# Kernel optimization log

Measured on AMD Instinct MI355X. Metric: run time of the kernel, lower is better.

Reference implementation:

```python
import jax, jax.numpy as jnp
import numpy as np

EPS = 1e-5

def gn(x, gamma, beta):
    # GroupNorm(num_groups=1) on [N, C]: normalize over channel dim per row
    m = x.mean(-1, keepdims=True)
    v = ((x - m) ** 2).mean(-1, keepdims=True)
    return (x - m) * jax.lax.rsqrt(v + EPS) * gamma + beta

def setup_inputs() -> dict:
    key = jax.random.key(0)
    N, M, E, D = 50000, 50000, 500000, 128
    ks = jax.random.split(key, 32)
    s = 0.05
    inp = {
        'agts': jax.random.normal(ks[0], (N, D), jnp.float32),
        'ctx': jax.random.normal(ks[1], (M, D), jnp.float32),
        'agt_ctrs': jax.random.normal(ks[2], (N, 2), jnp.float32),
        'ctx_ctrs': jax.random.normal(ks[3], (M, 2), jnp.float32),
        'hi': jax.random.randint(ks[4], (E,), 0, N, jnp.int32),
        'wi': jax.random.randint(ks[5], (E,), 0, M, jnp.int32),
        # dist MLP: Linear(2,D,bias) -> ReLU -> Linear(D,D,nobias)+GN+ReLU
        'W_d1': jax.random.normal(ks[6], (2, D), jnp.float32) * s,
        'b_d1': jnp.zeros((D,), jnp.float32),
        'W_d2': jax.random.normal(ks[7], (D, D), jnp.float32) * s,
        'g_d2': jnp.ones((D,), jnp.float32),
        'b_d2': jnp.zeros((D,), jnp.float32),
        # query: Linear(D,D,nobias)+GN+ReLU
        'W_q': jax.random.normal(ks[8], (D, D), jnp.float32) * s,
        'g_q': jnp.ones((D,), jnp.float32),
        'b_q': jnp.zeros((D,), jnp.float32),
        # ctx MLP: Linear(3D,D,nobias)+GN+ReLU -> Linear(D,D,nobias)
        'W_c1': jax.random.normal(ks[9], (3 * D, D), jnp.float32) * s,
        'g_c1': jnp.ones((D,), jnp.float32),
        'b_c1': jnp.zeros((D,), jnp.float32),
        'W_c2': jax.random.normal(ks[10], (D, D), jnp.float32) * s,
        # agt linear (nobias), post-scatter GN, final Linear(D,D,nobias)+GN (no act)
        'W_a': jax.random.normal(ks[11], (D, D), jnp.float32) * s,
        'g_n': jnp.ones((D,), jnp.float32),
        'b_n': jnp.zeros((D,), jnp.float32),
        'W_l': jax.random.normal(ks[12], (D, D), jnp.float32) * s,
        'g_l': jnp.ones((D,), jnp.float32),
        'b_l': jnp.zeros((D,), jnp.float32),
    }
    return inp

def reference(agts, ctx, agt_ctrs, ctx_ctrs, hi, wi,
              W_d1, b_d1, W_d2, g_d2, b_d2,
              W_q, g_q, b_q,
              W_c1, g_c1, b_c1, W_c2,
              W_a, g_n, b_n, W_l, g_l, b_l):
    res = agts
    # gather per-edge relative distances and embed
    dist = agt_ctrs[hi] - ctx_ctrs[wi]                      # [E, 2]
    d = jax.nn.relu(dist @ W_d1 + b_d1)                     # [E, D]
    d = jax.nn.relu(gn(d @ W_d2, g_d2, b_d2))               # [E, D]
    # per-edge agent query
    q = jax.nn.relu(gn(agts[hi] @ W_q, g_q, b_q))           # [E, D]
    # concat(dist_emb, query, gathered ctx) -> message MLP
    msg = jnp.concatenate([d, q, ctx[wi]], axis=-1)         # [E, 3D]
    msg = jax.nn.relu(gn(msg @ W_c1, g_c1, b_c1)) @ W_c2    # [E, D]
    # transform agents and scatter-add messages
    a = agts @ W_a
    a = a.at[hi].add(msg)
    a = jax.nn.relu(gn(a, g_n, b_n))
    a = gn(a @ W_l, g_l, b_l)   # act=False
    a = jax.nn.relu(a + res)
    return a
```

## Files before the change

### kernel.cpp

```cpp
#include <hip/hip_runtime.h>
#include <hip/hip_bf16.h>
#include <stdint.h>


typedef __bf16 bfx8 __attribute__((ext_vector_type(8)));
typedef float f32x4 __attribute__((ext_vector_type(4)));
typedef short s16x2 __attribute__((ext_vector_type(2)));

__device__ __forceinline__ unsigned short f2bfu(float f) {
  unsigned u = __builtin_bit_cast(unsigned, f);
  return (unsigned short)((u + 0x7fffu + ((u >> 16) & 1u)) >> 16);
}
__device__ __forceinline__ float bfu2f(unsigned short u) {
  return __builtin_bit_cast(float, ((unsigned)u) << 16);
}
__device__ __forceinline__ unsigned pk2(unsigned x, unsigned y) {
  float lo = bfu2f((unsigned short)(x & 0xffffu)) + bfu2f((unsigned short)(y & 0xffffu));
  float hi = bfu2f((unsigned short)(x >> 16)) + bfu2f((unsigned short)(y >> 16));
  return (unsigned)f2bfu(lo) | ((unsigned)f2bfu(hi) << 16);
}

__device__ __forceinline__ void atomAddBf2(unsigned short* p, unsigned v) {
#if defined(__has_builtin) && __has_builtin(__builtin_amdgcn_global_atomic_fadd_v2bf16)
  __builtin_amdgcn_global_atomic_fadd_v2bf16(
      (__attribute__((address_space(1))) s16x2*)p, __builtin_bit_cast(s16x2, v));
#else
  unsigned* q = (unsigned*)p;
  unsigned old = *q;
  while (true) {
    unsigned nv = pk2(old, v);
    unsigned prev = atomicCAS(q, old, nv);
    if (prev == old) break;
    old = prev;
  }
#endif
}

__device__ __forceinline__ int swzb(int row, int kbyte) {
  return (row * 256 + kbyte) ^ ((row & 7) << 4);
}

__device__ __forceinline__ void stage_w(const unsigned short* wsrc, char* dst, int tid, int nth) {
  const uint4* s = (const uint4*)wsrc;
  uint4* d = (uint4*)dst;
  for (int i = tid; i < 2048; i += nth) d[i] = s[i];
}

template <bool A_FROM_LDS>
__device__ __forceinline__ void wave_gemm(const char* WtL, const char* XL,
                                          const bfx8* aF, f32x4 acc[8],
                                          int lg, int lr) {
#pragma unroll
  for (int ks = 0; ks < 4; ++ks) {
    bfx8 a;
    if (A_FROM_LDS)
      a = *(const bfx8*)(XL + swzb(lr, (ks * 32 + lg * 8) * 2));
    else
      a = aF[ks];
#pragma unroll
    for (int t = 0; t < 8; ++t) {
      int n = t * 16 + lr;
      bfx8 b = *(const bfx8*)(WtL + swzb(n, (ks * 32 + lg * 8) * 2));
      acc[t] = __builtin_amdgcn_mfma_f32_16x16x32_bf16(a, b, acc[t], 0, 0, 0);
    }
  }
}

__device__ __forceinline__ void wave_gn(f32x4 acc[8], const float* g, const float* b,
                                        int lg, int lr, bool do_relu) {
  float s0 = 0.f, s1 = 0.f, s2 = 0.f, s3 = 0.f;
  float q0 = 0.f, q1 = 0.f, q2 = 0.f, q3 = 0.f;
#pragma unroll
  for (int t = 0; t < 8; ++t) {
    float v0 = acc[t][0], v1 = acc[t][1], v2 = acc[t][2], v3 = acc[t][3];
    s0 += v0; q0 += v0 * v0;
    s1 += v1; q1 += v1 * v1;
    s2 += v2; q2 += v2 * v2;
    s3 += v3; q3 += v3 * v3;
  }
#pragma unroll
  for (int m = 1; m <= 8; m <<= 1) {
    s0 += __shfl_xor(s0, m, 64); q0 += __shfl_xor(q0, m, 64);
    s1 += __shfl_xor(s1, m, 64); q1 += __shfl_xor(q1, m, 64);
    s2 += __shfl_xor(s2, m, 64); q2 += __shfl_xor(q2, m, 64);
    s3 += __shfl_xor(s3, m, 64); q3 += __shfl_xor(q3, m, 64);
  }
  float gc[8], bc[8];
#pragma unroll
  for (int t = 0; t < 8; ++t) { gc[t] = g[t * 16 + lr]; bc[t] = b[t * 16 + lr]; }
  float mean[4], rstd[4];
  {
    const float inv = 1.f / 128.f;
    float m0 = s0 * inv, m1 = s1 * inv, m2 = s2 * inv, m3 = s3 * inv;
    mean[0] = m0; mean[1] = m1; mean[2] = m2; mean[3] = m3;
    rstd[0] = rsqrtf(q0 * inv - m0 * m0 + 1e-5f);
    rstd[1] = rsqrtf(q1 * inv - m1 * m1 + 1e-5f);
    rstd[2] = rsqrtf(q2 * inv - m2 * m2 + 1e-5f);
    rstd[3] = rsqrtf(q3 * inv - m3 * m3 + 1e-5f);
  }
#pragma unroll
  for (int t = 0; t < 8; ++t) {
#pragma unroll
    for (int r = 0; r < 4; ++r) {
      float v = (acc[t][r] - mean[r]) * rstd[r] * gc[t] + bc[t];
      if (do_relu) v = fmaxf(v, 0.f);
      acc[t][r] = v;
    }
  }
}

__device__ __forceinline__ void wave_stage(char* XL, const f32x4 acc[8], int lg, int lr) {
#pragma unroll
  for (int t = 0; t < 8; ++t) {
#pragma unroll
    for (int r = 0; r < 4; ++r) {
      int row = 4 * lg + r, c = t * 16 + lr;
      *(unsigned short*)(XL + swzb(row, 2 * c)) = f2bfu(acc[t][r]);
    }
  }
}

__global__ void k_prep_weights(const float* Wd2, const float* Wc1, const float* Wc2,
                               const float* Wq, const float* Wa, const float* Wl,
                               unsigned short* wsW) {
  __shared__ unsigned short tmp[128 * 128];
  int m = blockIdx.x;
  const float* src;
  switch (m) {
    case 0: src = Wd2; break;
    case 1: src = Wc1; break;
    case 2: src = Wc1 + 128 * 128; break;
    case 3: src = Wc1 + 256 * 128; break;
    case 4: src = Wc2; break;
    case 5: src = Wq; break;
    case 6: src = Wa; break;
    default: src = Wl; break;
  }
  int tid = threadIdx.x;
#pragma unroll
  for (int i = 0; i < 16; ++i) {
    int lin = i * 256 + tid;
    float4 v = ((const float4*)src)[lin];
    ushort4 b;
    b.x = f2bfu(v.x); b.y = f2bfu(v.y); b.z = f2bfu(v.z); b.w = f2bfu(v.w);
    *(ushort4*)&tmp[lin * 4] = b;
  }
  __syncthreads();
  unsigned short* dst = wsW + (size_t)m * 16384;
#pragma unroll
  for (int i = 0; i < 16; ++i) {
    int lin = i * 256 + tid;
    int n = lin >> 5, q = lin & 31, k0 = q * 4;
    ushort4 b;
    b.x = tmp[(k0 + 0) * 128 + n];
    b.y = tmp[(k0 + 1) * 128 + n];
    b.z = tmp[(k0 + 2) * 128 + n];
    b.w = tmp[(k0 + 3) * 128 + n];
    *(ushort4*)((char*)dst + swzb(n, k0 * 2)) = b;
  }
}

__global__ void k_hist(const int* hi, int* cnt, int E) {
  int e = blockIdx.x * 256 + threadIdx.x;
  if (e < E) atomicAdd(&cnt[hi[e]], 1);
}

__global__ __launch_bounds__(1024) void k_scan(const int* cnt, int* cur, int N) {
  __shared__ int part[1024];
  int tid = threadIdx.x;
  int C = (N + 1023) >> 10;
  int b0 = tid * C, b1 = b0 + C; if (b1 > N) b1 = N; if (b0 > N) b0 = N;
  int s = 0;
  for (int i = b0; i < b1; ++i) s += cnt[i];
  part[tid] = s;
  __syncthreads();
  for (int d = 1; d < 1024; d <<= 1) {
    int v = (tid >= d) ? part[tid - d] : 0;
    __syncthreads();
    part[tid] += v;
    __syncthreads();
  }
  int excl = (tid == 0) ? 0 : part[tid - 1];
  for (int i = b0; i < b1; ++i) {
    cur[i] = excl;
    excl += cnt[i];
  }
}

__global__ void k_fill(const int* hi, const int* wi, int* cur,
                       int* hi_s, int* wi_s, int E) {
  int e = blockIdx.x * 256 + threadIdx.x;
  if (e < E) {
    int h = hi[e];
    int p = atomicAdd(&cur[h], 1);
    hi_s[p] = h;
    wi_s[p] = wi[e];
  }
}

__global__ __launch_bounds__(256, 2) void k_ctx(const float* ctx, const unsigned short* wsW,
                                                unsigned short* cc, int M) {
  __shared__ __align__(16) char lds[32768];
  int tid = threadIdx.x, wid = tid >> 6, lane = tid & 63, lg = lane >> 4, lr = lane & 15;
  int base = blockIdx.x * 64;
  stage_w(wsW + 3 * 16384, lds, tid, 256);
  int row = base + 16 * wid + lr;
  int rload = row < M ? row : M - 1;
  bfx8 cf[4];
#pragma unroll
  for (int ks = 0; ks < 4; ++ks) {
    int k0 = ks * 32 + lg * 8;
    const float4* p = (const float4*)&ctx[(size_t)rload * 128 + k0];
    float4 a = p[0], b = p[1];
    bfx8 f;
    f[0] = (__bf16)a.x; f[1] = (__bf16)a.y; f[2] = (__bf16)a.z; f[3] = (__bf16)a.w;
    f[4] = (__bf16)b.x; f[5] = (__bf16)b.y; f[6] = (__bf16)b.z; f[7] = (__bf16)b.w;
    cf[ks] = f;
  }
  __syncthreads();
  f32x4 acc[8];
#pragma unroll
  for (int t = 0; t < 8; ++t) acc[t] = 0.f;
  wave_gemm<false>(lds, nullptr, cf, acc, lg, lr);
#pragma unroll
  for (int r = 0; r < 4; ++r) {
    int grow = base + 16 * wid + 4 * lg + r;
    if (grow < M) {
#pragma unroll
      for (int t = 0; t < 8; ++t)
        cc[(size_t)grow * 128 + t * 16 + lr] = f2bfu(acc[t][r]);
    }
  }
}

__global__ __launch_bounds__(768, 3) void k_agents(const float* agts, const float* g_q,
                                                   const float* b_q, const unsigned short* wsW,
                                                   unsigned short* qc, int N) {
  __shared__ __align__(16) char lds[114688];
  char* WqL = lds;
  char* WcL = lds + 32768;
  int tid = threadIdx.x, wid = tid >> 6, lane = tid & 63, lg = lane >> 4, lr = lane & 15;
  char* actL = lds + 65536 + wid * 4096;
  stage_w(wsW + 5 * 16384, WqL, tid, 768);
  stage_w(wsW + 2 * 16384, WcL, tid, 768);
  __syncthreads();
  int nTiles = (N + 15) >> 4;
  int stride = gridDim.x * 12;
  for (int tile = blockIdx.x * 12 + wid; tile < nTiles; tile += stride) {
    int base = tile << 4;
    int row = base + lr; if (row >= N) row = N - 1;
    bfx8 af[4];
#pragma unroll
    for (int ks = 0; ks < 4; ++ks) {
      int k0 = ks * 32 + lg * 8;
      const float4* p = (const float4*)&agts[(size_t)row * 128 + k0];
      float4 a = p[0], b = p[1];
      bfx8 f;
      f[0] = (__bf16)a.x; f[1] = (__bf16)a.y; f[2] = (__bf16)a.z; f[3] = (__bf16)a.w;
      f[4] = (__bf16)b.x; f[5] = (__bf16)b.y; f[6] = (__bf16)b.z; f[7] = (__bf16)b.w;
      af[ks] = f;
    }
    f32x4 acc[8];
#pragma unroll
    for (int t = 0; t < 8; ++t) acc[t] = 0.f;
    wave_gemm<false>(WqL, nullptr, af, acc, lg, lr);
    wave_gn(acc, g_q, b_q, lg, lr, true);
    wave_stage(actL, acc, lg, lr);
#pragma unroll
    for (int t = 0; t < 8; ++t) acc[t] = 0.f;
    wave_gemm<true>(WcL, actL, nullptr, acc, lg, lr);
#pragma unroll
    for (int r = 0; r < 4; ++r) {
      int grow = base + 4 * lg + r;
      if (grow < N) {
#pragma unroll
        for (int t = 0; t < 8; ++t)
          qc[(size_t)grow * 128 + t * 16 + lr] = f2bfu(acc[t][r]);
      }
    }
  }
}

__global__ __launch_bounds__(768, 3) void k_edge(
    const float* agt_ctrs, const float* ctx_ctrs, const int* hi_s, const int* wi_s,
    const float* W_d1, const float* b_d1, const float* g_d2, const float* b_d2,
    const float* g_c1, const float* b_c1, const unsigned short* wsW,
    const unsigned short* qc, const unsigned short* cc, unsigned short* S, int E) {
  __shared__ __align__(16) char lds[163840];
  char* Wd2L = lds;
  char* Wc1L = lds + 32768;
  int tid = threadIdx.x, wid = tid >> 6, lane = tid & 63, lg = lane >> 4, lr = lane & 15;
  char* region = lds + 65536 + wid * 8192;
  char* QCCL = region;
  char* actL = region + 4096;
  float* hB = (float*)region;
  stage_w(wsW + 0 * 16384, Wd2L, tid, 768);
  stage_w(wsW + 1 * 16384, Wc1L, tid, 768);
  __syncthreads();
  int nTiles = (E + 15) >> 4;
  int stride = gridDim.x * 12;
  for (int tile = blockIdx.x * 12 + wid; tile < nTiles; tile += stride) {
    int base = tile << 4;
    {
      int gr = lane >> 2, gq = lane & 3;
      int ge = base + gr; if (ge >= E) ge = E - 1;
      int gh = hi_s[ge], gw2 = wi_s[ge];
      const uint4* qrow = (const uint4*)(qc + (size_t)gh * 128) + gq * 4;
      const uint4* crow = (const uint4*)(cc + (size_t)gw2 * 128) + gq * 4;
#pragma unroll
      for (int i = 0; i < 4; ++i) {
        uint4 av = qrow[i], bv = crow[i];
        uint4 o;
        o.x = pk2(av.x, bv.x); o.y = pk2(av.y, bv.y);
        o.z = pk2(av.z, bv.z); o.w = pk2(av.w, bv.w);
        *(uint4*)(QCCL + swzb(gr, gq * 64 + i * 16)) = o;
      }
    }
    bfx8 d1f[4];
    {
      int e1 = base + lr; if (e1 >= E) e1 = E - 1;
      int h1 = hi_s[e1], w1 = wi_s[e1];
      float dx = agt_ctrs[2 * h1] - ctx_ctrs[2 * w1];
      float dy = agt_ctrs[2 * h1 + 1] - ctx_ctrs[2 * w1 + 1];
#pragma unroll
      for (int ks = 0; ks < 4; ++ks) {
        int k0 = ks * 32 + lg * 8;
        const float4* w0 = (const float4*)&W_d1[k0];
        const float4* w1p = (const float4*)&W_d1[128 + k0];
        const float4* bp = (const float4*)&b_d1[k0];
        float4 w0a = w0[0], w0b = w0[1];
        float4 w1a = w1p[0], w1b = w1p[1];
        float4 ba = bp[0], bb = bp[1];
        bfx8 f;
        f[0] = (__bf16)fmaxf(dx * w0a.x + dy * w1a.x + ba.x, 0.f);
        f[1] = (__bf16)fmaxf(dx * w0a.y + dy * w1a.y + ba.y, 0.f);
        f[2] = (__bf16)fmaxf(dx * w0a.z + dy * w1a.z + ba.z, 0.f);
        f[3] = (__bf16)fmaxf(dx * w0a.w + dy * w1a.w + ba.w, 0.f);
        f[4] = (__bf16)fmaxf(dx * w0b.x + dy * w1b.x + bb.x, 0.f);
        f[5] = (__bf16)fmaxf(dx * w0b.y + dy * w1b.y + bb.y, 0.f);
        f[6] = (__bf16)fmaxf(dx * w0b.z + dy * w1b.z + bb.z, 0.f);
        f[7] = (__bf16)fmaxf(dx * w0b.w + dy * w1b.w + bb.w, 0.f);
        d1f[ks] = f;
      }
    }
    f32x4 acc[8];
#pragma unroll
    for (int t = 0; t < 8; ++t) acc[t] = 0.f;
    wave_gemm<false>(Wd2L, nullptr, d1f, acc, lg, lr);
    wave_gn(acc, g_d2, b_d2, lg, lr, true);
    wave_stage(actL, acc, lg, lr);
#pragma unroll
    for (int t = 0; t < 8; ++t) {
#pragma unroll
      for (int r = 0; r < 4; ++r)
        acc[t][r] = bfu2f(*(const unsigned short*)(QCCL + swzb(4 * lg + r, 2 * (16 * t + lr))));
    }
    wave_gemm<true>(Wc1L, actL, nullptr, acc, lg, lr);
    wave_gn(acc, g_c1, b_c1, lg, lr, true);
#pragma unroll
    for (int t = 0; t < 8; ++t) {
#pragma unroll
      for (int r = 0; r < 4; ++r)
        hB[(4 * lg + r) * 128 + 16 * t + lr] = acc[t][r];
    }
    {
      int nprev = (base > 0) ? hi_s[base - 1] : -1;
      int nnext = (base + 16 < E) ? hi_s[base + 16] : -1;
      int curn = -1, seg_start = 0;
      float s0 = 0.f, s1 = 0.f;
#pragma unroll
      for (int r = 0; r <= 16; ++r) {
        int n;
        if (r < 16) {
          int sl = base + r;
          n = (sl < E) ? hi_s[sl] : -1;
        } else {
          n = -2;
        }
        if (n != curn) {
          if (curn >= 0) {
            bool atomS = (seg_start == 0) && (curn == nprev);
            bool atomE = (r == 16) && (curn == nnext);
            unsigned pkv = (unsigned)f2bfu(s0) | ((unsigned)f2bfu(s1) << 16);
            unsigned short* addr = S + (size_t)curn * 128 + 2 * lane;
            if (atomS || atomE) atomAddBf2(addr, pkv);
            else *(unsigned*)addr = pkv;
          }
          curn = n; seg_start = r; s0 = 0.f; s1 = 0.f;
        }
        if (r < 16 && n >= 0) {
          float2 hv = *(const float2*)(hB + r * 128 + 2 * lane);
          s0 += hv.x; s1 += hv.y;
        }
      }
    }
  }
}

__global__ __launch_bounds__(768, 3) void k_final(const float* agts, const float* g_n,
                                                  const float* b_n, const float* g_l,
                                                  const float* b_l, const unsigned short* wsW,
                                                  const unsigned short* S, float* out, int N) {
  __shared__ __align__(16) char lds[147456];
  char* WaL = lds;
  char* Wc2L = lds + 32768;
  char* WlL = lds + 65536;
  int tid = threadIdx.x, wid = tid >> 6, lane = tid & 63, lg = lane >> 4, lr = lane & 15;
  char* actL = lds + 98304 + wid * 4096;
  stage_w(wsW + 6 * 16384, WaL, tid, 768);
  stage_w(wsW + 4 * 16384, Wc2L, tid, 768);
  stage_w(wsW + 7 * 16384, WlL, tid, 768);
  __syncthreads();
  int nTiles = (N + 15) >> 4;
  int stride = gridDim.x * 12;
  for (int tile = blockIdx.x * 12 + wid; tile < nTiles; tile += stride) {
    int base = tile << 4;
    int row = base + lr; if (row >= N) row = N - 1;
    bfx8 af[4], sf[4];
#pragma unroll
    for (int ks = 0; ks < 4; ++ks) {
      int k0 = ks * 32 + lg * 8;
      const float4* p = (const float4*)&agts[(size_t)row * 128 + k0];
      float4 a = p[0], b = p[1];
      bfx8 f;
      f[0] = (__bf16)a.x; f[1] = (__bf16)a.y; f[2] = (__bf16)a.z; f[3] = (__bf16)a.w;
      f[4] = (__bf16)b.x; f[5] = (__bf16)b.y; f[6] = (__bf16)b.z; f[7] = (__bf16)b.w;
      af[ks] = f;
      sf[ks] = *(const bfx8*)&S[(size_t)row * 128 + k0];
    }
    f32x4 acc[8];
#pragma unroll
    for (int t = 0; t < 8; ++t) acc[t] = 0.f;
    wave_gemm<false>(WaL, nullptr, af, acc, lg, lr);
    wave_gemm<false>(Wc2L, nullptr, sf, acc, lg, lr);
    wave_gn(acc, g_n, b_n, lg, lr, true);
    wave_stage(actL, acc, lg, lr);
#pragma unroll
    for (int t = 0; t < 8; ++t) acc[t] = 0.f;
    wave_gemm<true>(WlL, actL, nullptr, acc, lg, lr);
    wave_gn(acc, g_l, b_l, lg, lr, false);
#pragma unroll
    for (int r = 0; r < 4; ++r) {
      int grow = base + 4 * lg + r;
      if (grow < N) {
#pragma unroll
        for (int t = 0; t < 8; ++t) {
          int c = t * 16 + lr;
          float res = agts[(size_t)grow * 128 + c];
          out[(size_t)grow * 128 + c] = fmaxf(acc[t][r] + res, 0.f);
        }
      }
    }
  }
}

extern "C" void kernel_launch(void* const* d_in, const int* in_sizes, int n_in,
                              void* d_out, int out_size, void* d_ws, size_t ws_size,
                              hipStream_t stream) {
  const float* agts = (const float*)d_in[0];
  const float* ctx = (const float*)d_in[1];
  const float* agt_ctrs = (const float*)d_in[2];
  const float* ctx_ctrs = (const float*)d_in[3];
  const int* hi = (const int*)d_in[4];
  const int* wi = (const int*)d_in[5];
  const float* W_d1 = (const float*)d_in[6];
  const float* b_d1 = (const float*)d_in[7];
  const float* W_d2 = (const float*)d_in[8];
  const float* g_d2 = (const float*)d_in[9];
  const float* b_d2 = (const float*)d_in[10];
  const float* W_q = (const float*)d_in[11];
  const float* g_q = (const float*)d_in[12];
  const float* b_q = (const float*)d_in[13];
  const float* W_c1 = (const float*)d_in[14];
  const float* g_c1 = (const float*)d_in[15];
  const float* b_c1 = (const float*)d_in[16];
  const float* W_c2 = (const float*)d_in[17];
  const float* W_a = (const float*)d_in[18];
  const float* g_n = (const float*)d_in[19];
  const float* b_n = (const float*)d_in[20];
  const float* W_l = (const float*)d_in[21];
  const float* g_l = (const float*)d_in[22];
  const float* b_l = (const float*)d_in[23];

  int N = in_sizes[0] / 128;
  int M = in_sizes[1] / 128;
  int E = in_sizes[4];

  float* out = (float*)d_out;
  char* ws = (char*)d_ws;
  size_t o = 0;
  unsigned short* qcP = (unsigned short*)(ws + o); o += (size_t)N * 256;
  unsigned short* ccP = (unsigned short*)(ws + o); o += (size_t)M * 256;
  unsigned short* Sp  = (unsigned short*)(ws + o); o += (size_t)N * 256;
  unsigned short* wsW = (unsigned short*)(ws + o); o += 262144;
  int* cnt  = (int*)(ws + o); o += ((size_t)N * 4 + 255) & ~255ull;
  int* cur  = (int*)(ws + o); o += ((size_t)N * 4 + 255) & ~255ull;
  int* hi_s = (int*)(ws + o); o += ((size_t)E * 4 + 255) & ~255ull;
  int* wi_s = (int*)(ws + o); o += ((size_t)E * 4 + 255) & ~255ull;

  hipMemsetAsync(cnt, 0, (size_t)N * 4, stream);
  hipMemsetAsync(Sp, 0, (size_t)N * 256, stream);
  k_prep_weights<<<8, 256, 0, stream>>>(W_d2, W_c1, W_c2, W_q, W_a, W_l, wsW);
  k_hist<<<(E + 255) / 256, 256, 0, stream>>>(hi, cnt, E);
  k_scan<<<1, 1024, 0, stream>>>(cnt, cur, N);
  k_fill<<<(E + 255) / 256, 256, 0, stream>>>(hi, wi, cur, hi_s, wi_s, E);
  k_ctx<<<(M + 63) / 64, 256, 0, stream>>>(ctx, wsW, ccP, M);
  k_agents<<<256, 768, 0, stream>>>(agts, g_q, b_q, wsW, qcP, N);
  k_edge<<<256, 768, 0, stream>>>(agt_ctrs, ctx_ctrs, hi_s, wi_s, W_d1, b_d1,
                                  g_d2, b_d2, g_c1, b_c1, wsW, qcP, ccP, Sp, E);
  k_final<<<256, 768, 0, stream>>>(agts, g_n, b_n, g_l, b_l, wsW, Sp, out, N);
}
```

Measured before the change: 363.5 us.

## Parallelize CSR scan, pack edge indices, and widen kernels to 1024 threads

Replaces the single-block serial scan with a three-pass multi-block scan and records per-edge ranks during the histogram. The fill step then writes sorted (h,w) pairs with plain stores instead of atomics. All main kernels move to 1024-thread blocks, and k_ctx becomes persistent. k_edge now gathers q/c values directly into registers instead of staging them through LDS, and hoists W_d1/b_d1 and the GN gamma/beta into registers once per block. The goal is to remove the serial scan bottleneck and LDS round-trips, at the cost of higher register pressure and the LDS footprint implied by the 4-blocks-per-CU launch bounds.

```diff
diff --git a/kernel.cpp b/kernel.cpp
--- a/kernel.cpp
+++ b/kernel.cpp
@@ -66,8 +66,14 @@
   }
 }
 
-__device__ __forceinline__ void wave_gn(f32x4 acc[8], const float* g, const float* b,
-                                        int lg, int lr, bool do_relu) {
+__device__ __forceinline__ void gn_cols(const float* __restrict__ g, const float* __restrict__ b,
+                                        int lr, float gc[8], float bc[8]) {
+#pragma unroll
+  for (int t = 0; t < 8; ++t) { gc[t] = g[t * 16 + lr]; bc[t] = b[t * 16 + lr]; }
+}
+
+__device__ __forceinline__ void wave_gn(f32x4 acc[8], const float gc[8], const float bc[8],
+                                        bool do_relu) {
   float s0 = 0.f, s1 = 0.f, s2 = 0.f, s3 = 0.f;
   float q0 = 0.f, q1 = 0.f, q2 = 0.f, q3 = 0.f;
 #pragma unroll
@@ -85,9 +91,6 @@
     s2 += __shfl_xor(s2, m, 64); q2 += __shfl_xor(q2, m, 64);
     s3 += __shfl_xor(s3, m, 64); q3 += __shfl_xor(q3, m, 64);
   }
-  float gc[8], bc[8];
-#pragma unroll
-  for (int t = 0; t < 8; ++t) { gc[t] = g[t * 16 + lr]; bc[t] = b[t * 16 + lr]; }
   float mean[4], rstd[4];
   {
     const float inv = 1.f / 128.f;
@@ -160,93 +163,133 @@
   }
 }
 
-__global__ void k_hist(const int* hi, int* cnt, int E) {
+__global__ void k_hist(const int* __restrict__ hi, int* cnt, int* rank, int E) {
   int e = blockIdx.x * 256 + threadIdx.x;
-  if (e < E) atomicAdd(&cnt[hi[e]], 1);
-}
-
-__global__ __launch_bounds__(1024) void k_scan(const int* cnt, int* cur, int N) {
-  __shared__ int part[1024];
-  int tid = threadIdx.x;
-  int C = (N + 1023) >> 10;
-  int b0 = tid * C, b1 = b0 + C; if (b1 > N) b1 = N; if (b0 > N) b0 = N;
+  if (e < E) rank[e] = atomicAdd(&cnt[hi[e]], 1);
+}
+
+__global__ void k_scan1(const int* __restrict__ cnt, int* bsum, int N) {
+  __shared__ int red[256];
+  int b = blockIdx.x, t = threadIdx.x;
+  int i0 = b * 1024 + t * 4;
   int s = 0;
-  for (int i = b0; i < b1; ++i) s += cnt[i];
-  part[tid] = s;
+#pragma unroll
+  for (int j = 0; j < 4; ++j) { int i = i0 + j; if (i < N) s += cnt[i]; }
+  red[t] = s;
+  __syncthreads();
+  for (int d = 128; d > 0; d >>= 1) {
+    if (t < d) red[t] += red[t + d];
+    __syncthreads();
+  }
+  if (t == 0) bsum[b] = red[0];
+}
+
+__global__ __launch_bounds__(1024) void k_scan2(int* bsum, int nb) {
+  __shared__ int sh[1024];
+  int t = threadIdx.x;
+  sh[t] = (t < nb) ? bsum[t] : 0;
   __syncthreads();
   for (int d = 1; d < 1024; d <<= 1) {
-    int v = (tid >= d) ? part[tid - d] : 0;
+    int v = (t >= d) ? sh[t - d] : 0;
     __syncthreads();
-    part[tid] += v;
+    sh[t] += v;
     __syncthreads();
   }
-  int excl = (tid == 0) ? 0 : part[tid - 1];
-  for (int i = b0; i < b1; ++i) {
-    cur[i] = excl;
-    excl += cnt[i];
-  }
-}
-
-__global__ void k_fill(const int* hi, const int* wi, int* cur,
-                       int* hi_s, int* wi_s, int E) {
+  if (t < nb) bsum[t] = (t == 0) ? 0 : sh[t - 1];
+}
+
+__global__ void k_scan3(const int* __restrict__ cnt, const int* __restrict__ bsum,
+                        int* base, int N) {
+  __shared__ int tsum[256];
+  int b = blockIdx.x, t = threadIdx.x;
+  int i0 = b * 1024 + t * 4;
+  int v[4]; int s = 0;
+#pragma unroll
+  for (int j = 0; j < 4; ++j) { int i = i0 + j; v[j] = (i < N) ? cnt[i] : 0; s += v[j]; }
+  tsum[t] = s;
+  __syncthreads();
+  for (int d = 1; d < 256; d <<= 1) {
+    int x = (t >= d) ? tsum[t - d] : 0;
+    __syncthreads();
+    tsum[t] += x;
+    __syncthreads();
+  }
+  int off = bsum[b] + ((t == 0) ? 0 : tsum[t - 1]);
+#pragma unroll
+  for (int j = 0; j < 4; ++j) {
+    int i = i0 + j;
+    if (i < N) { base[i] = off; off += v[j]; }
+  }
+}
+
+__global__ void k_fill(const int* __restrict__ hi, const int* __restrict__ wi,
+                       const int* __restrict__ base, const int* __restrict__ rank,
+                       uint2* hw, int E) {
   int e = blockIdx.x * 256 + threadIdx.x;
   if (e < E) {
     int h = hi[e];
-    int p = atomicAdd(&cur[h], 1);
-    hi_s[p] = h;
-    wi_s[p] = wi[e];
-  }
-}
-
-__global__ __launch_bounds__(256, 2) void k_ctx(const float* ctx, const unsigned short* wsW,
-                                                unsigned short* cc, int M) {
+    int p = base[h] + rank[e];
+    hw[p] = make_uint2((unsigned)h, (unsigned)wi[e]);
+  }
+}
+
+__global__ __launch_bounds__(1024, 4) void k_ctx(const float* __restrict__ ctx,
+                                                 const unsigned short* __restrict__ wsW,
+                                                 unsigned short* __restrict__ cc, int M) {
   __shared__ __align__(16) char lds[32768];
   int tid = threadIdx.x, wid = tid >> 6, lane = tid & 63, lg = lane >> 4, lr = lane & 15;
-  int base = blockIdx.x * 64;
-  stage_w(wsW + 3 * 16384, lds, tid, 256);
-  int row = base + 16 * wid + lr;
-  int rload = row < M ? row : M - 1;
-  bfx8 cf[4];
-#pragma unroll
-  for (int ks = 0; ks < 4; ++ks) {
-    int k0 = ks * 32 + lg * 8;
-    const float4* p = (const float4*)&ctx[(size_t)rload * 128 + k0];
-    float4 a = p[0], b = p[1];
-    bfx8 f;
-    f[0] = (__bf16)a.x; f[1] = (__bf16)a.y; f[2] = (__bf16)a.z; f[3] = (__bf16)a.w;
-    f[4] = (__bf16)b.x; f[5] = (__bf16)b.y; f[6] = (__bf16)b.z; f[7] = (__bf16)b.w;
-    cf[ks] = f;
-  }
-  __syncthreads();
-  f32x4 acc[8];
-#pragma unroll
-  for (int t = 0; t < 8; ++t) acc[t] = 0.f;
-  wave_gemm<false>(lds, nullptr, cf, acc, lg, lr);
-#pragma unroll
-  for (int r = 0; r < 4; ++r) {
-    int grow = base + 16 * wid + 4 * lg + r;
-    if (grow < M) {
-#pragma unroll
-      for (int t = 0; t < 8; ++t)
-        cc[(size_t)grow * 128 + t * 16 + lr] = f2bfu(acc[t][r]);
-    }
-  }
-}
-
-__global__ __launch_bounds__(768, 3) void k_agents(const float* agts, const float* g_q,
-                                                   const float* b_q, const unsigned short* wsW,
-                                                   unsigned short* qc, int N) {
-  __shared__ __align__(16) char lds[114688];
+  stage_w(wsW + 3 * 16384, lds, tid, 1024);
+  __syncthreads();
+  int nTiles = (M + 15) >> 4;
+  int stride = gridDim.x * 16;
+  for (int tile = blockIdx.x * 16 + wid; tile < nTiles; tile += stride) {
+    int base = tile << 4;
+    int row = base + lr; if (row >= M) row = M - 1;
+    bfx8 cf[4];
+#pragma unroll
+    for (int ks = 0; ks < 4; ++ks) {
+      int k0 = ks * 32 + lg * 8;
+      const float4* p = (const float4*)&ctx[(size_t)row * 128 + k0];
+      float4 a = p[0], b = p[1];
+      bfx8 f;
+      f[0] = (__bf16)a.x; f[1] = (__bf16)a.y; f[2] = (__bf16)a.z; f[3] = (__bf16)a.w;
+      f[4] = (__bf16)b.x; f[5] = (__bf16)b.y; f[6] = (__bf16)b.z; f[7] = (__bf16)b.w;
+      cf[ks] = f;
+    }
+    f32x4 acc[8];
+#pragma unroll
+    for (int t = 0; t < 8; ++t) acc[t] = 0.f;
+    wave_gemm<false>(lds, nullptr, cf, acc, lg, lr);
+#pragma unroll
+    for (int r = 0; r < 4; ++r) {
+      int grow = base + 4 * lg + r;
+      if (grow < M) {
+#pragma unroll
+        for (int t = 0; t < 8; ++t)
+          cc[(size_t)grow * 128 + t * 16 + lr] = f2bfu(acc[t][r]);
+      }
+    }
+  }
+}
+
+__global__ __launch_bounds__(1024, 4) void k_agents(const float* __restrict__ agts,
+                                                    const float* __restrict__ g_q,
+                                                    const float* __restrict__ b_q,
+                                                    const unsigned short* __restrict__ wsW,
+                                                    unsigned short* __restrict__ qc, int N) {
+  __shared__ __align__(16) char lds[131072];
   char* WqL = lds;
   char* WcL = lds + 32768;
   int tid = threadIdx.x, wid = tid >> 6, lane = tid & 63, lg = lane >> 4, lr = lane & 15;
   char* actL = lds + 65536 + wid * 4096;
-  stage_w(wsW + 5 * 16384, WqL, tid, 768);
-  stage_w(wsW + 2 * 16384, WcL, tid, 768);
+  stage_w(wsW + 5 * 16384, WqL, tid, 1024);
+  stage_w(wsW + 2 * 16384, WcL, tid, 1024);
+  float gq[8], bq[8];
+  gn_cols(g_q, b_q, lr, gq, bq);
   __syncthreads();
   int nTiles = (N + 15) >> 4;
-  int stride = gridDim.x * 12;
-  for (int tile = blockIdx.x * 12 + wid; tile < nTiles; tile += stride) {
+  int stride = gridDim.x * 16;
+  for (int tile = blockIdx.x * 16 + wid; tile < nTiles; tile += stride) {
     int base = tile << 4;
     int row = base + lr; if (row >= N) row = N - 1;
     bfx8 af[4];
@@ -264,7 +307,7 @@
 #pragma unroll
     for (int t = 0; t < 8; ++t) acc[t] = 0.f;
     wave_gemm<false>(WqL, nullptr, af, acc, lg, lr);
-    wave_gn(acc, g_q, b_q, lg, lr, true);
+    wave_gn(acc, gq, bq, true);
     wave_stage(actL, acc, lg, lr);
 #pragma unroll
     for (int t = 0; t < 8; ++t) acc[t] = 0.f;
@@ -281,139 +324,141 @@
   }
 }
 
-__global__ __launch_bounds__(768, 3) void k_edge(
-    const float* agt_ctrs, const float* ctx_ctrs, const int* hi_s, const int* wi_s,
-    const float* W_d1, const float* b_d1, const float* g_d2, const float* b_d2,
-    const float* g_c1, const float* b_c1, const unsigned short* wsW,
-    const unsigned short* qc, const unsigned short* cc, unsigned short* S, int E) {
-  __shared__ __align__(16) char lds[163840];
+__global__ __launch_bounds__(1024, 4) void k_edge(
+    const float* __restrict__ agt_ctrs, const float* __restrict__ ctx_ctrs,
+    const uint2* __restrict__ hw,
+    const float* __restrict__ W_d1, const float* __restrict__ b_d1,
+    const float* __restrict__ g_d2, const float* __restrict__ b_d2,
+    const float* __restrict__ g_c1, const float* __restrict__ b_c1,
+    const unsigned short* __restrict__ wsW,
+    const unsigned short* __restrict__ qc, const unsigned short* __restrict__ cc,
+    unsigned short* __restrict__ S, int E) {
+  __shared__ __align__(16) char lds[131072];
   char* Wd2L = lds;
   char* Wc1L = lds + 32768;
   int tid = threadIdx.x, wid = tid >> 6, lane = tid & 63, lg = lane >> 4, lr = lane & 15;
-  char* region = lds + 65536 + wid * 8192;
-  char* QCCL = region;
-  char* actL = region + 4096;
-  float* hB = (float*)region;
-  stage_w(wsW + 0 * 16384, Wd2L, tid, 768);
-  stage_w(wsW + 1 * 16384, Wc1L, tid, 768);
+  char* actL = lds + 65536 + wid * 4096;
+  stage_w(wsW + 0 * 16384, Wd2L, tid, 1024);
+  stage_w(wsW + 1 * 16384, Wc1L, tid, 1024);
+  float wda[4][8], wdb[4][8], wdc[4][8];
+#pragma unroll
+  for (int ks = 0; ks < 4; ++ks) {
+    int k0 = ks * 32 + lg * 8;
+    float4 a0 = *(const float4*)&W_d1[k0], a1 = *(const float4*)&W_d1[k0 + 4];
+    float4 b0 = *(const float4*)&W_d1[128 + k0], b1 = *(const float4*)&W_d1[128 + k0 + 4];
+    float4 c0 = *(const float4*)&b_d1[k0], c1 = *(const float4*)&b_d1[k0 + 4];
+    wda[ks][0] = a0.x; wda[ks][1] = a0.y; wda[ks][2] = a0.z; wda[ks][3] = a0.w;
+    wda[ks][4] = a1.x; wda[ks][5] = a1.y; wda[ks][6] = a1.z; wda[ks][7] = a1.w;
+    wdb[ks][0] = b0.x; wdb[ks][1] = b0.y; wdb[ks][2] = b0.z; wdb[ks][3] = b0.w;
+    wdb[ks][4] = b1.x; wdb[ks][5] = b1.y; wdb[ks][6] = b1.z; wdb[ks][7] = b1.w;
+    wdc[ks][0] = c0.x; wdc[ks][1] = c0.y; wdc[ks][2] = c0.z; wdc[ks][3] = c0.w;
+    wdc[ks][4] = c1.x; wdc[ks][5] = c1.y; wdc[ks][6] = c1.z; wdc[ks][7] = c1.w;
+  }
+  float gd[8], bd[8], gc1c[8], bc1c[8];
+  gn_cols(g_d2, b_d2, lr, gd, bd);
+  gn_cols(g_c1, b_c1, lr, gc1c, bc1c);
   __syncthreads();
   int nTiles = (E + 15) >> 4;
-  int stride = gridDim.x * 12;
-  for (int tile = blockIdx.x * 12 + wid; tile < nTiles; tile += stride) {
+  int stride = gridDim.x * 16;
+  for (int tile = blockIdx.x * 16 + wid; tile < nTiles; tile += stride) {
     int base = tile << 4;
+    int er = base + lr;
+    bool val = er < E;
+    int erc = val ? er : E - 1;
+    uint2 hwv = hw[erc];
+    int h = (int)hwv.x, w = (int)hwv.y;
+    int nprev = (base > 0) ? (int)hw[base - 1].x : -1;
+    int nnext = (base + 16 < E) ? (int)hw[base + 16].x : -1;
+    unsigned short qv[8][4], cv[8][4];
+#pragma unroll
+    for (int r = 0; r < 4; ++r) {
+      int hr = __shfl(h, 4 * lg + r, 64);
+      int wr = __shfl(w, 4 * lg + r, 64);
+      const unsigned short* qp = qc + (size_t)hr * 128 + lr;
+      const unsigned short* cp = cc + (size_t)wr * 128 + lr;
+#pragma unroll
+      for (int t = 0; t < 8; ++t) { qv[t][r] = qp[t * 16]; cv[t][r] = cp[t * 16]; }
+    }
+    float dx, dy;
     {
-      int gr = lane >> 2, gq = lane & 3;
-      int ge = base + gr; if (ge >= E) ge = E - 1;
-      int gh = hi_s[ge], gw2 = wi_s[ge];
-      const uint4* qrow = (const uint4*)(qc + (size_t)gh * 128) + gq * 4;
-      const uint4* crow = (const uint4*)(cc + (size_t)gw2 * 128) + gq * 4;
-#pragma unroll
-      for (int i = 0; i < 4; ++i) {
-        uint4 av = qrow[i], bv = crow[i];
-        uint4 o;
-        o.x = pk2(av.x, bv.x); o.y = pk2(av.y, bv.y);
-        o.z = pk2(av.z, bv.z); o.w = pk2(av.w, bv.w);
-        *(uint4*)(QCCL + swzb(gr, gq * 64 + i * 16)) = o;
-      }
+      float2 ac = *(const float2*)&agt_ctrs[2 * h];
+      float2 cx = *(const float2*)&ctx_ctrs[2 * w];
+      dx = ac.x - cx.x; dy = ac.y - cx.y;
     }
     bfx8 d1f[4];
-    {
-      int e1 = base + lr; if (e1 >= E) e1 = E - 1;
-      int h1 = hi_s[e1], w1 = wi_s[e1];
-      float dx = agt_ctrs[2 * h1] - ctx_ctrs[2 * w1];
-      float dy = agt_ctrs[2 * h1 + 1] - ctx_ctrs[2 * w1 + 1];
-#pragma unroll
-      for (int ks = 0; ks < 4; ++ks) {
-        int k0 = ks * 32 + lg * 8;
-        const float4* w0 = (const float4*)&W_d1[k0];
-        const float4* w1p = (const float4*)&W_d1[128 + k0];
-        const float4* bp = (const float4*)&b_d1[k0];
-        float4 w0a = w0[0], w0b = w0[1];
-        float4 w1a = w1p[0], w1b = w1p[1];
-        float4 ba = bp[0], bb = bp[1];
-        bfx8 f;
-        f[0] = (__bf16)fmaxf(dx * w0a.x + dy * w1a.x + ba.x, 0.f);
-        f[1] = (__bf16)fmaxf(dx * w0a.y + dy * w1a.y + ba.y, 0.f);
-        f[2] = (__bf16)fmaxf(dx * w0a.z + dy * w1a.z + ba.z, 0.f);
-        f[3] = (__bf16)fmaxf(dx * w0a.w + dy * w1a.w + ba.w, 0.f);
-        f[4] = (__bf16)fmaxf(dx * w0b.x + dy * w1b.x + bb.x, 0.f);
-        f[5] = (__bf16)fmaxf(dx * w0b.y + dy * w1b.y + bb.y, 0.f);
-        f[6] = (__bf16)fmaxf(dx * w0b.z + dy * w1b.z + bb.z, 0.f);
-        f[7] = (__bf16)fmaxf(dx * w0b.w + dy * w1b.w + bb.w, 0.f);
-        d1f[ks] = f;
-      }
+#pragma unroll
+    for (int ks = 0; ks < 4; ++ks) {
+      bfx8 f;
+#pragma unroll
+      for (int j = 0; j < 8; ++j)
+        f[j] = (__bf16)fmaxf(dx * wda[ks][j] + dy * wdb[ks][j] + wdc[ks][j], 0.f);
+      d1f[ks] = f;
     }
     f32x4 acc[8];
 #pragma unroll
     for (int t = 0; t < 8; ++t) acc[t] = 0.f;
     wave_gemm<false>(Wd2L, nullptr, d1f, acc, lg, lr);
-    wave_gn(acc, g_d2, b_d2, lg, lr, true);
+    wave_gn(acc, gd, bd, true);
     wave_stage(actL, acc, lg, lr);
 #pragma unroll
     for (int t = 0; t < 8; ++t) {
 #pragma unroll
       for (int r = 0; r < 4; ++r)
-        acc[t][r] = bfu2f(*(const unsigned short*)(QCCL + swzb(4 * lg + r, 2 * (16 * t + lr))));
+        acc[t][r] = bfu2f(qv[t][r]) + bfu2f(cv[t][r]);
     }
     wave_gemm<true>(Wc1L, actL, nullptr, acc, lg, lr);
-    wave_gn(acc, g_c1, b_c1, lg, lr, true);
-#pragma unroll
-    for (int t = 0; t < 8; ++t) {
-#pragma unroll
-      for (int r = 0; r < 4; ++r)
-        hB[(4 * lg + r) * 128 + 16 * t + lr] = acc[t][r];
-    }
-    {
-      int nprev = (base > 0) ? hi_s[base - 1] : -1;
-      int nnext = (base + 16 < E) ? hi_s[base + 16] : -1;
-      int curn = -1, seg_start = 0;
-      float s0 = 0.f, s1 = 0.f;
-#pragma unroll
-      for (int r = 0; r <= 16; ++r) {
-        int n;
-        if (r < 16) {
-          int sl = base + r;
-          n = (sl < E) ? hi_s[sl] : -1;
-        } else {
-          n = -2;
+    wave_gn(acc, gc1c, bc1c, true);
+    wave_stage(actL, acc, lg, lr);
+    int nmy = val ? h : -1;
+    float s0 = 0.f, s1 = 0.f;
+    int curn = -1, seg_start = 0;
+#pragma unroll
+    for (int r = 0; r <= 16; ++r) {
+      int n = (r < 16) ? __shfl(nmy, r, 64) : -2;
+      if (n != curn) {
+        if (curn >= 0) {
+          bool aS = (seg_start == 0) && (curn == nprev);
+          bool aE = (r == 16) && (curn == nnext);
+          unsigned pkv = (unsigned)f2bfu(s0) | ((unsigned)f2bfu(s1) << 16);
+          unsigned short* addr = S + (size_t)curn * 128 + 2 * lane;
+          if (aS || aE) atomAddBf2(addr, pkv);
+          else *(unsigned*)addr = pkv;
         }
-        if (n != curn) {
-          if (curn >= 0) {
-            bool atomS = (seg_start == 0) && (curn == nprev);
-            bool atomE = (r == 16) && (curn == nnext);
-            unsigned pkv = (unsigned)f2bfu(s0) | ((unsigned)f2bfu(s1) << 16);
-            unsigned short* addr = S + (size_t)curn * 128 + 2 * lane;
-            if (atomS || atomE) atomAddBf2(addr, pkv);
-            else *(unsigned*)addr = pkv;
-          }
-          curn = n; seg_start = r; s0 = 0.f; s1 = 0.f;
-        }
-        if (r < 16 && n >= 0) {
-          float2 hv = *(const float2*)(hB + r * 128 + 2 * lane);
-          s0 += hv.x; s1 += hv.y;
-        }
+        curn = n; seg_start = r; s0 = 0.f; s1 = 0.f;
       }
-    }
-  }
-}
-
-__global__ __launch_bounds__(768, 3) void k_final(const float* agts, const float* g_n,
-                                                  const float* b_n, const float* g_l,
-                                                  const float* b_l, const unsigned short* wsW,
-                                                  const unsigned short* S, float* out, int N) {
-  __shared__ __align__(16) char lds[147456];
+      if (r < 16 && n >= 0) {
+        unsigned hv = *(const unsigned*)(actL + swzb(r, 4 * lane));
+        s0 += bfu2f((unsigned short)(hv & 0xffffu));
+        s1 += bfu2f((unsigned short)(hv >> 16));
+      }
+    }
+  }
+}
+
+__global__ __launch_bounds__(1024, 4) void k_final(const float* __restrict__ agts,
+                                                   const float* __restrict__ g_n,
+                                                   const float* __restrict__ b_n,
+                                                   const float* __restrict__ g_l,
+                                                   const float* __restrict__ b_l,
+                                                   const unsigned short* __restrict__ wsW,
+                                                   const unsigned short* __restrict__ S,
+                                                   float* __restrict__ out, int N) {
+  __shared__ __align__(16) char lds[163840];
   char* WaL = lds;
   char* Wc2L = lds + 32768;
   char* WlL = lds + 65536;
   int tid = threadIdx.x, wid = tid >> 6, lane = tid & 63, lg = lane >> 4, lr = lane & 15;
   char* actL = lds + 98304 + wid * 4096;
-  stage_w(wsW + 6 * 16384, WaL, tid, 768);
-  stage_w(wsW + 4 * 16384, Wc2L, tid, 768);
-  stage_w(wsW + 7 * 16384, WlL, tid, 768);
+  stage_w(wsW + 6 * 16384, WaL, tid, 1024);
+  stage_w(wsW + 4 * 16384, Wc2L, tid, 1024);
+  stage_w(wsW + 7 * 16384, WlL, tid, 1024);
+  float gn8[8], bn8[8], gl8[8], bl8[8];
+  gn_cols(g_n, b_n, lr, gn8, bn8);
+  gn_cols(g_l, b_l, lr, gl8, bl8);
   __syncthreads();
   int nTiles = (N + 15) >> 4;
-  int stride = gridDim.x * 12;
-  for (int tile = blockIdx.x * 12 + wid; tile < nTiles; tile += stride) {
+  int stride = gridDim.x * 16;
+  for (int tile = blockIdx.x * 16 + wid; tile < nTiles; tile += stride) {
     int base = tile << 4;
     int row = base + lr; if (row >= N) row = N - 1;
     bfx8 af[4], sf[4];
@@ -433,12 +478,12 @@
     for (int t = 0; t < 8; ++t) acc[t] = 0.f;
     wave_gemm<false>(WaL, nullptr, af, acc, lg, lr);
     wave_gemm<false>(Wc2L, nullptr, sf, acc, lg, lr);
-    wave_gn(acc, g_n, b_n, lg, lr, true);
+    wave_gn(acc, gn8, bn8, true);
     wave_stage(actL, acc, lg, lr);
 #pragma unroll
     for (int t = 0; t < 8; ++t) acc[t] = 0.f;
     wave_gemm<true>(WlL, actL, nullptr, acc, lg, lr);
-    wave_gn(acc, g_l, b_l, lg, lr, false);
+    wave_gn(acc, gl8, bl8, false);
 #pragma unroll
     for (int r = 0; r < 4; ++r) {
       int grow = base + 4 * lg + r;
@@ -494,19 +539,24 @@
   unsigned short* Sp  = (unsigned short*)(ws + o); o += (size_t)N * 256;
   unsigned short* wsW = (unsigned short*)(ws + o); o += 262144;
   int* cnt  = (int*)(ws + o); o += ((size_t)N * 4 + 255) & ~255ull;
-  int* cur  = (int*)(ws + o); o += ((size_t)N * 4 + 255) & ~255ull;
-  int* hi_s = (int*)(ws + o); o += ((size_t)E * 4 + 255) & ~255ull;
-  int* wi_s = (int*)(ws + o); o += ((size_t)E * 4 + 255) & ~255ull;
+  int* baseA= (int*)(ws + o); o += ((size_t)N * 4 + 255) & ~255ull;
+  int* rank = (int*)(ws + o); o += ((size_t)E * 4 + 255) & ~255ull;
+  int* bsum = (int*)(ws + o); o += 8192;
+  uint2* hwP = (uint2*)(ws + o); o += ((size_t)E * 8 + 255) & ~255ull;
+
+  int nb = (N + 1023) / 1024;
 
   hipMemsetAsync(cnt, 0, (size_t)N * 4, stream);
   hipMemsetAsync(Sp, 0, (size_t)N * 256, stream);
   k_prep_weights<<<8, 256, 0, stream>>>(W_d2, W_c1, W_c2, W_q, W_a, W_l, wsW);
-  k_hist<<<(E + 255) / 256, 256, 0, stream>>>(hi, cnt, E);
-  k_scan<<<1, 1024, 0, stream>>>(cnt, cur, N);
-  k_fill<<<(E + 255) / 256, 256, 0, stream>>>(hi, wi, cur, hi_s, wi_s, E);
-  k_ctx<<<(M + 63) / 64, 256, 0, stream>>>(ctx, wsW, ccP, M);
-  k_agents<<<256, 768, 0, stream>>>(agts, g_q, b_q, wsW, qcP, N);
-  k_edge<<<256, 768, 0, stream>>>(agt_ctrs, ctx_ctrs, hi_s, wi_s, W_d1, b_d1,
-                                  g_d2, b_d2, g_c1, b_c1, wsW, qcP, ccP, Sp, E);
-  k_final<<<256, 768, 0, stream>>>(agts, g_n, b_n, g_l, b_l, wsW, Sp, out, N);
-}
+  k_hist<<<(E + 255) / 256, 256, 0, stream>>>(hi, cnt, rank, E);
+  k_scan1<<<nb, 256, 0, stream>>>(cnt, bsum, N);
+  k_scan2<<<1, 1024, 0, stream>>>(bsum, nb);
+  k_scan3<<<nb, 256, 0, stream>>>(cnt, bsum, baseA, N);
+  k_fill<<<(E + 255) / 256, 256, 0, stream>>>(hi, wi, baseA, rank, hwP, E);
+  k_ctx<<<256, 1024, 0, stream>>>(ctx, wsW, ccP, M);
+  k_agents<<<256, 1024, 0, stream>>>(agts, g_q, b_q, wsW, qcP, N);
+  k_edge<<<256, 1024, 0, stream>>>(agt_ctrs, ctx_ctrs, hwP, W_d1, b_d1,
+                                   g_d2, b_d2, g_c1, b_c1, wsW, qcP, ccP, Sp, E);
+  k_final<<<256, 1024, 0, stream>>>(agts, g_n, b_n, g_l, b_l, wsW, Sp, out, N);
+}
```

Result: slower. 705.6 us (+94.1%).
